# Optimization experiments

Hardware: AMD Instinct MI355X
Metric: run time of the kernel (lower is better)

Reference implementation:

```python
import jax, jax.numpy as jnp
import numpy as np

B, N, DEG, DIN, DM, H, DH, DO = 8, 4096, 16, 64, 128, 4, 32, 32
NLAYERS = 3
NN_SCALE = 1999853.335557038


def _layernorm(x, g, b, eps=1e-5):
    mu = jnp.mean(x, axis=-1, keepdims=True)
    var = jnp.var(x, axis=-1, keepdims=True)
    return (x - mu) * jax.lax.rsqrt(var + eps) * g + b


def setup_inputs() -> dict:
    key = jax.random.key(0)
    ks = jax.random.split(key, 24)
    s = 0.1
    inp = {
        'node_features': jax.random.normal(ks[0], (B, N, DIN), jnp.float32),
        'query_idxs': jax.random.randint(ks[1], (B,), 0, N, jnp.int32),
        'masks': (jax.random.uniform(ks[2], (B, N, DEG, 1)) > 0.2).astype(jnp.float32),
        'adj': jax.random.randint(ks[3], (B, N, DEG), 0, N, jnp.int32),
        'sim_results': jax.random.normal(ks[4], (B, 8), jnp.float32),
        'W0': jax.random.normal(ks[5], (DIN, DM), jnp.float32) * s,
        'b0': jnp.zeros((DM,), jnp.float32),
        'Wl': jax.random.normal(ks[6], (NLAYERS, H, DM, DH), jnp.float32) * s,
        'a_src': jax.random.normal(ks[7], (NLAYERS, H, DH), jnp.float32) * s,
        'a_dst': jax.random.normal(ks[8], (NLAYERS, H, DH), jnp.float32) * s,
        'Wo': jax.random.normal(ks[9], (NLAYERS, H, DH, DO), jnp.float32) * s,
        'Wlin': jax.random.normal(ks[10], (NLAYERS, H * DO, DM), jnp.float32) * s,
        'blin': jnp.zeros((NLAYERS, DM), jnp.float32),
        'ln_g': jnp.ones((NLAYERS, DM), jnp.float32),
        'ln_b': jnp.zeros((NLAYERS, DM), jnp.float32),
        'Wf1': jax.random.normal(ks[11], (DM, 256), jnp.float32) * s,
        'bf1': jnp.zeros((256,), jnp.float32),
        'Wf2': jax.random.normal(ks[12], (256, 128), jnp.float32) * s,
        'bf2': jnp.zeros((128,), jnp.float32),
        'Wf3': jax.random.normal(ks[13], (128, 8), jnp.float32) * s,
        'bf3': jnp.zeros((8,), jnp.float32),
    }
    return inp


def reference(node_features, query_idxs, masks, adj, sim_results,
              W0, b0, Wl, a_src, a_dst, Wo, Wlin, blin, ln_g, ln_b,
              Wf1, bf1, Wf2, bf2, Wf3, bf3):
    elu = jax.nn.elu
    x = elu(node_features @ W0 + b0)  # (B, N, DM)
    idx = adj.reshape(B, N * DEG, 1, 1)  # gather indices along node axis
    valid = masks > 0  # (B, N, DEG, 1)
    for l in range(NLAYERS):
        h = jnp.einsum('bnd,hdk->bnhk', x, Wl[l])  # (B, N, H, DH)
        hn = jnp.take_along_axis(h, idx, axis=1).reshape(B, N, DEG, H, DH)
        e_src = jnp.einsum('bnhk,hk->bnh', h, a_src[l])  # (B, N, H)
        e_dst = jnp.einsum('bnmhk,hk->bnmh', hn, a_dst[l])  # (B, N, DEG, H)
        e = jax.nn.leaky_relu(e_src[:, :, None, :] + e_dst, 0.2)
        e = jnp.where(valid, e, -1e9)
        alpha = jax.nn.softmax(e, axis=2)  # over neighbors
        agg = jnp.einsum('bnmh,bnmhk->bnhk', alpha, hn)  # (B, N, H, DH)
        out = jnp.einsum('bnhk,hko->bnho', agg, Wo[l]).reshape(B, N, H * DO)
        out = elu(out @ Wlin[l] + blin[l])  # AttnModule linear + ELU
        x = _layernorm(out + x, ln_g[l], ln_b[l])  # residual + LN
    qi = query_idxs.reshape(B, 1, 1)
    vnf = jnp.take_along_axis(x, qi, axis=1)[:, 0, :]  # (B, DM)
    vnf = elu(vnf @ Wf1 + bf1)
    vnf = elu(vnf @ Wf2 + bf2)
    vnf = elu(vnf @ Wf3 + bf3)
    return vnf * NN_SCALE
```

## Files before the change

### kernel.cpp

```cpp
#include <hip/hip_runtime.h>
#include <hip/hip_bf16.h>
#include <math.h>

#define BATCH 8
#define NNODE 4096
#define DEG 16
#define DIN 64
#define DM 128
#define NH 4
#define DHD 32
#define BN (BATCH*NNODE)
#define NLAYERS 3
#define NN_SCALE 1999853.335557038f

#define X_OFF     0
#define H_OFF     (BN*DM)
#define AGG_OFF   (2*BN*DM)
#define WLP_OFF   (3*BN*DM)
#define WCOMB_OFF (WLP_OFF + NLAYERS*DM*DM)

__device__ __forceinline__ float elu_f(float x) {
  return x > 0.f ? x : expm1f(x);
}

__global__ __launch_bounds__(256) void prep_kernel(
    const float* __restrict__ Wl, const float* __restrict__ Wo,
    const float* __restrict__ Wlin, float* __restrict__ ws) {
  const int bid = blockIdx.x;
  const int l = bid >> 4, sl = bid & 15;
  float* Wlp = ws + WLP_OFF   + l*DM*DM;
  float* Wcb = ws + WCOMB_OFF + l*DM*DM;
  const float* Wl_l   = Wl   + l*NH*DM*DHD;
  const float* Wo_l   = Wo   + l*NH*DHD*DHD;
  const float* Wlin_l = Wlin + l*DM*DM;
  for (int idx = sl*1024 + threadIdx.x; idx < (sl+1)*1024; idx += 256) {
    int d = idx >> 7, c = idx & 127;
    Wlp[idx] = Wl_l[((c>>5)*DM + d)*DHD + (c&31)];
  }
  for (int idx = sl*1024 + threadIdx.x; idx < (sl+1)*1024; idx += 256) {
    int r = idx >> 7, dcol = idx & 127;
    int h = r >> 5, k = r & 31;
    const float* wo  = Wo_l + (h*DHD + k)*DHD;
    const float* wl2 = Wlin_l + (h*DHD)*DM + dcol;
    float acc = 0.f;
    #pragma unroll
    for (int o = 0; o < DHD; o++) acc = fmaf(wo[o], wl2[o*DM], acc);
    Wcb[idx] = acc;
  }
}

template<int K, int EPI>
__global__ __launch_bounds__(128) void gemm_kernel(
    const float* __restrict__ A, const float* __restrict__ W,
    const float* __restrict__ bias, const float* __restrict__ lng,
    const float* __restrict__ lnb, const float* __restrict__ res,
    float* __restrict__ out) {
  __shared__ float xT[32][36];
  __shared__ float Wc[32][132];
  const int tid = threadIdx.x;
  const int j = tid & 15, i = tid >> 4;
  const int bid  = blockIdx.x;
  const int row0 = ((bid & 7) * 128 + (bid >> 3)) * 32;

  float acc[4][8];
  #pragma unroll
  for (int a = 0; a < 4; a++)
    #pragma unroll
    for (int b = 0; b < 8; b++) acc[a][b] = 0.f;

  float bval[8], gv[8], bv2[8];
  if (EPI != 0) {
    #pragma unroll
    for (int cc = 0; cc < 8; cc++) bval[cc] = bias[j*8 + cc];
  }
  if (EPI == 2) {
    #pragma unroll
    for (int cc = 0; cc < 8; cc++) { gv[cc] = lng[j*8+cc]; bv2[cc] = lnb[j*8+cc]; }
  }

  const int kq = tid & 7, rb = tid >> 3;

  float4 aR[2], wR[8];
  #pragma unroll
  for (int p = 0; p < 2; p++)
    aR[p] = *reinterpret_cast<const float4*>(
        &A[(size_t)(row0 + rb + p*16)*K + kq*4]);
  #pragma unroll
  for (int p = 0; p < 8; p++) {
    const int idx = p*128 + tid;
    const int d = idx >> 5, cq = idx & 31;
    wR[p] = *reinterpret_cast<const float4*>(&W[(size_t)d*128 + cq*4]);
  }

  for (int k0 = 0; k0 < K; k0 += 32) {
    __syncthreads();
    #pragma unroll
    for (int p = 0; p < 2; p++) {
      const int r = rb + p*16;
      xT[kq*4+0][r] = aR[p].x; xT[kq*4+1][r] = aR[p].y;
      xT[kq*4+2][r] = aR[p].z; xT[kq*4+3][r] = aR[p].w;
    }
    #pragma unroll
    for (int p = 0; p < 8; p++) {
      const int idx = p*128 + tid;
      const int d = idx >> 5, cq = idx & 31;
      *reinterpret_cast<float4*>(&Wc[d][cq*4]) = wR[p];
    }
    __syncthreads();
    if (k0 + 32 < K) {
      #pragma unroll
      for (int p = 0; p < 2; p++)
        aR[p] = *reinterpret_cast<const float4*>(
            &A[(size_t)(row0 + rb + p*16)*K + (k0 + 32) + kq*4]);
      #pragma unroll
      for (int p = 0; p < 8; p++) {
        const int idx = p*128 + tid;
        const int d = idx >> 5, cq = idx & 31;
        wR[p] = *reinterpret_cast<const float4*>(
            &W[(size_t)(k0 + 32 + d)*128 + cq*4]);
      }
    }
    #pragma unroll
    for (int kk = 0; kk < 32; kk++) {
      const float4 a0 = *reinterpret_cast<const float4*>(&xT[kk][i*4]);
      const float av[4] = {a0.x, a0.y, a0.z, a0.w};
      const float4 w0 = *reinterpret_cast<const float4*>(&Wc[kk][j*8]);
      const float4 w1 = *reinterpret_cast<const float4*>(&Wc[kk][j*8+4]);
      const float wv[8] = {w0.x,w0.y,w0.z,w0.w,w1.x,w1.y,w1.z,w1.w};
      #pragma unroll
      for (int rr = 0; rr < 4; rr++)
        #pragma unroll
        for (int cc = 0; cc < 8; cc++)
          acc[rr][cc] = fmaf(av[rr], wv[cc], acc[rr][cc]);
    }
  }

  if (EPI == 0) {
    #pragma unroll
    for (int rr = 0; rr < 4; rr++) {
      float* op = out + (size_t)(row0 + i*4 + rr)*DM + j*8;
      float4 v0 = {acc[rr][0],acc[rr][1],acc[rr][2],acc[rr][3]};
      float4 v1 = {acc[rr][4],acc[rr][5],acc[rr][6],acc[rr][7]};
      *reinterpret_cast<float4*>(op)     = v0;
      *reinterpret_cast<float4*>(op + 4) = v1;
    }
  } else if (EPI == 1) {
    #pragma unroll
    for (int rr = 0; rr < 4; rr++) {
      float* op = out + (size_t)(row0 + i*4 + rr)*DM + j*8;
      float4 v0, v1;
      v0.x = elu_f(acc[rr][0]+bval[0]); v0.y = elu_f(acc[rr][1]+bval[1]);
      v0.z = elu_f(acc[rr][2]+bval[2]); v0.w = elu_f(acc[rr][3]+bval[3]);
      v1.x = elu_f(acc[rr][4]+bval[4]); v1.y = elu_f(acc[rr][5]+bval[5]);
      v1.z = elu_f(acc[rr][6]+bval[6]); v1.w = elu_f(acc[rr][7]+bval[7]);
      *reinterpret_cast<float4*>(op)     = v0;
      *reinterpret_cast<float4*>(op + 4) = v1;
    }
  } else {
    float s[4], s2[4];
    #pragma unroll
    for (int rr = 0; rr < 4; rr++) {
      const int r = row0 + i*4 + rr;
      const float4 r0 = *reinterpret_cast<const float4*>(&res[(size_t)r*DM + j*8]);
      const float4 r1 = *reinterpret_cast<const float4*>(&res[(size_t)r*DM + j*8 + 4]);
      const float rv[8] = {r0.x,r0.y,r0.z,r0.w,r1.x,r1.y,r1.z,r1.w};
      s[rr] = 0.f; s2[rr] = 0.f;
      #pragma unroll
      for (int cc = 0; cc < 8; cc++) {
        float v = elu_f(acc[rr][cc] + bval[cc]) + rv[cc];
        acc[rr][cc] = v; s[rr] += v; s2[rr] += v*v;
      }
    }
    #pragma unroll
    for (int o = 1; o < 16; o <<= 1) {
      #pragma unroll
      for (int rr = 0; rr < 4; rr++) {
        s[rr]  += __shfl_xor(s[rr],  o);
        s2[rr] += __shfl_xor(s2[rr], o);
      }
    }
    #pragma unroll
    for (int rr = 0; rr < 4; rr++) {
      const int r = row0 + i*4 + rr;
      const float mu  = s[rr] * (1.f/128.f);
      const float var = s2[rr] * (1.f/128.f) - mu*mu;
      const float rs  = rsqrtf(var + 1e-5f);
      float4 v0, v1;
      v0.x = (acc[rr][0]-mu)*rs*gv[0] + bv2[0];
      v0.y = (acc[rr][1]-mu)*rs*gv[1] + bv2[1];
      v0.z = (acc[rr][2]-mu)*rs*gv[2] + bv2[2];
      v0.w = (acc[rr][3]-mu)*rs*gv[3] + bv2[3];
      v1.x = (acc[rr][4]-mu)*rs*gv[4] + bv2[4];
      v1.y = (acc[rr][5]-mu)*rs*gv[5] + bv2[5];
      v1.z = (acc[rr][6]-mu)*rs*gv[6] + bv2[6];
      v1.w = (acc[rr][7]-mu)*rs*gv[7] + bv2[7];
      float* op = out + (size_t)r*DM + j*8;
      *reinterpret_cast<float4*>(op)     = v0;
      *reinterpret_cast<float4*>(op + 4) = v1;
    }
  }
}

__global__ __launch_bounds__(256) void attn_kernel(
    const float* __restrict__ h, const int* __restrict__ adj,
    const float* __restrict__ masks, const float* __restrict__ a_src,
    const float* __restrict__ a_dst, float* __restrict__ agg) {
  const int lane = threadIdx.x & 63;
  const int wid  = threadIdx.x >> 6;
  const int bid  = blockIdx.x;
  const int node = ((bid & 7) << 12) + ((bid >> 3) << 2) + wid;
  const int b    = node >> 12;
  const int half = lane >> 5;
  const int c    = lane & 31;

  const float4 asr4 = *reinterpret_cast<const float4*>(a_src + 4*c);
  const float4 ad4  = *reinterpret_cast<const float4*>(a_dst + 4*c);

  const float4 hv = *reinterpret_cast<const float4*>(h + (size_t)node*DM + 4*c);
  float es = hv.x*asr4.x + hv.y*asr4.y + hv.z*asr4.z + hv.w*asr4.w;
  es += __shfl_xor(es, 1); es += __shfl_xor(es, 2); es += __shfl_xor(es, 4);

  float4 v[8]; float e[8];
  #pragma unroll
  for (int i = 0; i < 8; i++) {
    const int m  = 2*i + half;
    const int jn = adj[node*DEG + m];
    const float mval = masks[node*DEG + m];
    v[i] = *reinterpret_cast<const float4*>(
        h + ((size_t)(b*NNODE + jn))*DM + 4*c);
    float ed = v[i].x*ad4.x + v[i].y*ad4.y + v[i].z*ad4.z + v[i].w*ad4.w;
    ed += __shfl_xor(ed, 1); ed += __shfl_xor(ed, 2); ed += __shfl_xor(ed, 4);
    float t = es + ed;
    t = t > 0.f ? t : 0.2f*t;
    e[i] = (mval > 0.f) ? t : -1e9f;
  }

  float mx = e[0];
  #pragma unroll
  for (int i = 1; i < 8; i++) mx = fmaxf(mx, e[i]);
  mx = fmaxf(mx, __shfl_xor(mx, 32));
  float s = 0.f;
  #pragma unroll
  for (int i = 0; i < 8; i++) { e[i] = __expf(e[i] - mx); s += e[i]; }
  s += __shfl_xor(s, 32);
  const float inv = 1.f / s;

  float4 acc = {0.f, 0.f, 0.f, 0.f};
  #pragma unroll
  for (int i = 0; i < 8; i++) {
    const float a = e[i] * inv;
    acc.x = fmaf(a, v[i].x, acc.x); acc.y = fmaf(a, v[i].y, acc.y);
    acc.z = fmaf(a, v[i].z, acc.z); acc.w = fmaf(a, v[i].w, acc.w);
  }
  acc.x += __shfl_xor(acc.x, 32); acc.y += __shfl_xor(acc.y, 32);
  acc.z += __shfl_xor(acc.z, 32); acc.w += __shfl_xor(acc.w, 32);

  if (half == 0)
    *reinterpret_cast<float4*>(agg + (size_t)node*DM + 4*c) = acc;
}

__global__ __launch_bounds__(256) void mlp_kernel(
    const float* __restrict__ x, const int* __restrict__ qidx,
    const float* __restrict__ Wf1, const float* __restrict__ bf1,
    const float* __restrict__ Wf2, const float* __restrict__ bf2,
    const float* __restrict__ Wf3, const float* __restrict__ bf3,
    float* __restrict__ out) {
  __shared__ float xv[128];
  __shared__ float y1[256];
  __shared__ float y2[128];
  const int b = blockIdx.x, t = threadIdx.x;
  const int qi = qidx[b];
  if (t < 128) xv[t] = x[((size_t)b*NNODE + qi)*DM + t];
  __syncthreads();
  {
    float a1 = bf1[t];
    #pragma unroll 8
    for (int d = 0; d < 128; d++) a1 = fmaf(xv[d], Wf1[d*256 + t], a1);
    y1[t] = elu_f(a1);
  }
  __syncthreads();
  if (t < 128) {
    float a2 = bf2[t];
    #pragma unroll 8
    for (int d = 0; d < 256; d++) a2 = fmaf(y1[d], Wf2[d*128 + t], a2);
    y2[t] = elu_f(a2);
  }
  __syncthreads();
  if (t < 8) {
    float a3 = bf3[t];
    #pragma unroll 8
    for (int d = 0; d < 128; d++) a3 = fmaf(y2[d], Wf3[d*8 + t], a3);
    out[b*8 + t] = elu_f(a3) * NN_SCALE;
  }
}

extern "C" void kernel_launch(void* const* d_in, const int* in_sizes, int n_in,
                              void* d_out, int out_size, void* d_ws, size_t ws_size,
                              hipStream_t stream) {
  (void)in_sizes; (void)n_in; (void)out_size; (void)ws_size;
  const float* nf    = (const float*)d_in[0];
  const int*   qidx  = (const int*)d_in[1];
  const float* masks = (const float*)d_in[2];
  const int*   adj   = (const int*)d_in[3];
  const float* W0    = (const float*)d_in[5];
  const float* b0    = (const float*)d_in[6];
  const float* Wl    = (const float*)d_in[7];
  const float* a_src = (const float*)d_in[8];
  const float* a_dst = (const float*)d_in[9];
  const float* Wo    = (const float*)d_in[10];
  const float* Wlin  = (const float*)d_in[11];
  const float* blin  = (const float*)d_in[12];
  const float* ln_g  = (const float*)d_in[13];
  const float* ln_b  = (const float*)d_in[14];
  const float* Wf1   = (const float*)d_in[15];
  const float* bf1   = (const float*)d_in[16];
  const float* Wf2   = (const float*)d_in[17];
  const float* bf2   = (const float*)d_in[18];
  const float* Wf3   = (const float*)d_in[19];
  const float* bf3   = (const float*)d_in[20];

  float* ws  = (float*)d_ws;
  float* x   = ws + X_OFF;
  float* h   = ws + H_OFF;
  float* agg = ws + AGG_OFF;

  prep_kernel<<<48, 256, 0, stream>>>(Wl, Wo, Wlin, ws);

  gemm_kernel<DIN, 1><<<BN/32, 128, 0, stream>>>(
      nf, W0, b0, nullptr, nullptr, nullptr, x);

  for (int l = 0; l < NLAYERS; l++) {
    const float* Wlp = ws + WLP_OFF   + l*DM*DM;
    const float* Wcb = ws + WCOMB_OFF + l*DM*DM;
    gemm_kernel<DM, 0><<<BN/32, 128, 0, stream>>>(
        x, Wlp, nullptr, nullptr, nullptr, nullptr, h);
    attn_kernel<<<BN/4, 256, 0, stream>>>(
        h, adj, masks, a_src + l*NH*DHD, a_dst + l*NH*DHD, agg);
    gemm_kernel<DM, 2><<<BN/32, 128, 0, stream>>>(
        agg, Wcb, blin + l*DM, ln_g + l*DM, ln_b + l*DM, x, x);
  }

  mlp_kernel<<<8, 256, 0, stream>>>(
      x, qidx, Wf1, bf1, Wf2, bf2, Wf3, bf3, (float*)d_out);
}
```

Measured before the change: 402.5 us.

## Fuse attention aggregation with output GEMM, residual and layernorm

```diff
diff --git a/kernel.cpp b/kernel.cpp
--- a/kernel.cpp
+++ b/kernel.cpp
@@ -15,8 +15,7 @@
 
 #define X_OFF     0
 #define H_OFF     (BN*DM)
-#define AGG_OFF   (2*BN*DM)
-#define WLP_OFF   (3*BN*DM)
+#define WLP_OFF   (2*BN*DM)
 #define WCOMB_OFF (WLP_OFF + NLAYERS*DM*DM)
 
 __device__ __forceinline__ float elu_f(float x) {
@@ -52,9 +51,7 @@
 template<int K, int EPI>
 __global__ __launch_bounds__(128) void gemm_kernel(
     const float* __restrict__ A, const float* __restrict__ W,
-    const float* __restrict__ bias, const float* __restrict__ lng,
-    const float* __restrict__ lnb, const float* __restrict__ res,
-    float* __restrict__ out) {
+    const float* __restrict__ bias, float* __restrict__ out) {
   __shared__ float xT[32][36];
   __shared__ float Wc[32][132];
   const int tid = threadIdx.x;
@@ -68,14 +65,10 @@
     #pragma unroll
     for (int b = 0; b < 8; b++) acc[a][b] = 0.f;
 
-  float bval[8], gv[8], bv2[8];
+  float bval[8];
   if (EPI != 0) {
     #pragma unroll
     for (int cc = 0; cc < 8; cc++) bval[cc] = bias[j*8 + cc];
-  }
-  if (EPI == 2) {
-    #pragma unroll
-    for (int cc = 0; cc < 8; cc++) { gv[cc] = lng[j*8+cc]; bv2[cc] = lnb[j*8+cc]; }
   }
 
   const int kq = tid & 7, rb = tid >> 3;
@@ -135,128 +128,174 @@
     }
   }
 
-  if (EPI == 0) {
-    #pragma unroll
-    for (int rr = 0; rr < 4; rr++) {
-      float* op = out + (size_t)(row0 + i*4 + rr)*DM + j*8;
-      float4 v0 = {acc[rr][0],acc[rr][1],acc[rr][2],acc[rr][3]};
-      float4 v1 = {acc[rr][4],acc[rr][5],acc[rr][6],acc[rr][7]};
-      *reinterpret_cast<float4*>(op)     = v0;
-      *reinterpret_cast<float4*>(op + 4) = v1;
-    }
-  } else if (EPI == 1) {
-    #pragma unroll
-    for (int rr = 0; rr < 4; rr++) {
-      float* op = out + (size_t)(row0 + i*4 + rr)*DM + j*8;
-      float4 v0, v1;
+  #pragma unroll
+  for (int rr = 0; rr < 4; rr++) {
+    float* op = out + (size_t)(row0 + i*4 + rr)*DM + j*8;
+    float4 v0, v1;
+    if (EPI == 0) {
+      v0 = make_float4(acc[rr][0],acc[rr][1],acc[rr][2],acc[rr][3]);
+      v1 = make_float4(acc[rr][4],acc[rr][5],acc[rr][6],acc[rr][7]);
+    } else {
       v0.x = elu_f(acc[rr][0]+bval[0]); v0.y = elu_f(acc[rr][1]+bval[1]);
       v0.z = elu_f(acc[rr][2]+bval[2]); v0.w = elu_f(acc[rr][3]+bval[3]);
       v1.x = elu_f(acc[rr][4]+bval[4]); v1.y = elu_f(acc[rr][5]+bval[5]);
       v1.z = elu_f(acc[rr][6]+bval[6]); v1.w = elu_f(acc[rr][7]+bval[7]);
-      *reinterpret_cast<float4*>(op)     = v0;
-      *reinterpret_cast<float4*>(op + 4) = v1;
-    }
-  } else {
-    float s[4], s2[4];
-    #pragma unroll
-    for (int rr = 0; rr < 4; rr++) {
-      const int r = row0 + i*4 + rr;
-      const float4 r0 = *reinterpret_cast<const float4*>(&res[(size_t)r*DM + j*8]);
-      const float4 r1 = *reinterpret_cast<const float4*>(&res[(size_t)r*DM + j*8 + 4]);
-      const float rv[8] = {r0.x,r0.y,r0.z,r0.w,r1.x,r1.y,r1.z,r1.w};
-      s[rr] = 0.f; s2[rr] = 0.f;
-      #pragma unroll
-      for (int cc = 0; cc < 8; cc++) {
-        float v = elu_f(acc[rr][cc] + bval[cc]) + rv[cc];
-        acc[rr][cc] = v; s[rr] += v; s2[rr] += v*v;
-      }
-    }
-    #pragma unroll
-    for (int o = 1; o < 16; o <<= 1) {
-      #pragma unroll
-      for (int rr = 0; rr < 4; rr++) {
-        s[rr]  += __shfl_xor(s[rr],  o);
-        s2[rr] += __shfl_xor(s2[rr], o);
-      }
-    }
-    #pragma unroll
-    for (int rr = 0; rr < 4; rr++) {
-      const int r = row0 + i*4 + rr;
-      const float mu  = s[rr] * (1.f/128.f);
-      const float var = s2[rr] * (1.f/128.f) - mu*mu;
-      const float rs  = rsqrtf(var + 1e-5f);
-      float4 v0, v1;
-      v0.x = (acc[rr][0]-mu)*rs*gv[0] + bv2[0];
-      v0.y = (acc[rr][1]-mu)*rs*gv[1] + bv2[1];
-      v0.z = (acc[rr][2]-mu)*rs*gv[2] + bv2[2];
-      v0.w = (acc[rr][3]-mu)*rs*gv[3] + bv2[3];
-      v1.x = (acc[rr][4]-mu)*rs*gv[4] + bv2[4];
-      v1.y = (acc[rr][5]-mu)*rs*gv[5] + bv2[5];
-      v1.z = (acc[rr][6]-mu)*rs*gv[6] + bv2[6];
-      v1.w = (acc[rr][7]-mu)*rs*gv[7] + bv2[7];
-      float* op = out + (size_t)r*DM + j*8;
-      *reinterpret_cast<float4*>(op)     = v0;
-      *reinterpret_cast<float4*>(op + 4) = v1;
-    }
-  }
-}
-
-__global__ __launch_bounds__(256) void attn_kernel(
+    }
+    *reinterpret_cast<float4*>(op)     = v0;
+    *reinterpret_cast<float4*>(op + 4) = v1;
+  }
+}
+
+__global__ __launch_bounds__(256) void fused_attn_out_kernel(
     const float* __restrict__ h, const int* __restrict__ adj,
     const float* __restrict__ masks, const float* __restrict__ a_src,
-    const float* __restrict__ a_dst, float* __restrict__ agg) {
-  const int lane = threadIdx.x & 63;
-  const int wid  = threadIdx.x >> 6;
+    const float* __restrict__ a_dst, const float* __restrict__ Wcb,
+    const float* __restrict__ blin, const float* __restrict__ lng,
+    const float* __restrict__ lnb, float* __restrict__ x) {
+  __shared__ float agg_s[32][132];
+  __shared__ float Wc[32][132];
+  const int tid  = threadIdx.x;
   const int bid  = blockIdx.x;
-  const int node = ((bid & 7) << 12) + ((bid >> 3) << 2) + wid;
-  const int b    = node >> 12;
-  const int half = lane >> 5;
-  const int c    = lane & 31;
-
-  const float4 asr4 = *reinterpret_cast<const float4*>(a_src + 4*c);
-  const float4 ad4  = *reinterpret_cast<const float4*>(a_dst + 4*c);
-
-  const float4 hv = *reinterpret_cast<const float4*>(h + (size_t)node*DM + 4*c);
-  float es = hv.x*asr4.x + hv.y*asr4.y + hv.z*asr4.z + hv.w*asr4.w;
-  es += __shfl_xor(es, 1); es += __shfl_xor(es, 2); es += __shfl_xor(es, 4);
-
-  float4 v[8]; float e[8];
-  #pragma unroll
-  for (int i = 0; i < 8; i++) {
-    const int m  = 2*i + half;
-    const int jn = adj[node*DEG + m];
-    const float mval = masks[node*DEG + m];
-    v[i] = *reinterpret_cast<const float4*>(
-        h + ((size_t)(b*NNODE + jn))*DM + 4*c);
-    float ed = v[i].x*ad4.x + v[i].y*ad4.y + v[i].z*ad4.z + v[i].w*ad4.w;
-    ed += __shfl_xor(ed, 1); ed += __shfl_xor(ed, 2); ed += __shfl_xor(ed, 4);
-    float t = es + ed;
-    t = t > 0.f ? t : 0.2f*t;
-    e[i] = (mval > 0.f) ? t : -1e9f;
-  }
-
-  float mx = e[0];
-  #pragma unroll
-  for (int i = 1; i < 8; i++) mx = fmaxf(mx, e[i]);
-  mx = fmaxf(mx, __shfl_xor(mx, 32));
-  float s = 0.f;
-  #pragma unroll
-  for (int i = 0; i < 8; i++) { e[i] = __expf(e[i] - mx); s += e[i]; }
-  s += __shfl_xor(s, 32);
-  const float inv = 1.f / s;
-
-  float4 acc = {0.f, 0.f, 0.f, 0.f};
-  #pragma unroll
-  for (int i = 0; i < 8; i++) {
-    const float a = e[i] * inv;
-    acc.x = fmaf(a, v[i].x, acc.x); acc.y = fmaf(a, v[i].y, acc.y);
-    acc.z = fmaf(a, v[i].z, acc.z); acc.w = fmaf(a, v[i].w, acc.w);
-  }
-  acc.x += __shfl_xor(acc.x, 32); acc.y += __shfl_xor(acc.y, 32);
-  acc.z += __shfl_xor(acc.z, 32); acc.w += __shfl_xor(acc.w, 32);
-
-  if (half == 0)
-    *reinterpret_cast<float4*>(agg + (size_t)node*DM + 4*c) = acc;
+  const int node0 = ((bid & 7) * 128 + (bid >> 3)) * 32;
+  const int b     = node0 >> 12;
+
+  {
+    const int lane = tid & 63;
+    const int wid  = tid >> 6;
+    const int half = lane >> 5;
+    const int c    = lane & 31;
+    const float4 asr4 = *reinterpret_cast<const float4*>(a_src + 4*c);
+    const float4 ad4  = *reinterpret_cast<const float4*>(a_dst + 4*c);
+
+    for (int it = 0; it < 8; ++it) {
+      const int nl   = wid*8 + it;
+      const int node = node0 + nl;
+
+      const float4 hv = *reinterpret_cast<const float4*>(
+          h + (size_t)node*DM + 4*c);
+      float es = hv.x*asr4.x + hv.y*asr4.y + hv.z*asr4.z + hv.w*asr4.w;
+      es += __shfl_xor(es, 1); es += __shfl_xor(es, 2); es += __shfl_xor(es, 4);
+
+      float4 v[8]; float e[8];
+      #pragma unroll
+      for (int i = 0; i < 8; i++) {
+        const int m  = 2*i + half;
+        const int jn = adj[node*DEG + m];
+        const float mval = masks[node*DEG + m];
+        v[i] = *reinterpret_cast<const float4*>(
+            h + ((size_t)(b*NNODE + jn))*DM + 4*c);
+        float ed = v[i].x*ad4.x + v[i].y*ad4.y + v[i].z*ad4.z + v[i].w*ad4.w;
+        ed += __shfl_xor(ed, 1); ed += __shfl_xor(ed, 2); ed += __shfl_xor(ed, 4);
+        float t = es + ed;
+        t = t > 0.f ? t : 0.2f*t;
+        e[i] = (mval > 0.f) ? t : -1e9f;
+      }
+
+      float mx = e[0];
+      #pragma unroll
+      for (int i = 1; i < 8; i++) mx = fmaxf(mx, e[i]);
+      mx = fmaxf(mx, __shfl_xor(mx, 32));
+      float s = 0.f;
+      #pragma unroll
+      for (int i = 0; i < 8; i++) { e[i] = __expf(e[i] - mx); s += e[i]; }
+      s += __shfl_xor(s, 32);
+      const float inv = 1.f / s;
+
+      float4 acc = {0.f, 0.f, 0.f, 0.f};
+      #pragma unroll
+      for (int i = 0; i < 8; i++) {
+        const float a = e[i] * inv;
+        acc.x = fmaf(a, v[i].x, acc.x); acc.y = fmaf(a, v[i].y, acc.y);
+        acc.z = fmaf(a, v[i].z, acc.z); acc.w = fmaf(a, v[i].w, acc.w);
+      }
+      acc.x += __shfl_xor(acc.x, 32); acc.y += __shfl_xor(acc.y, 32);
+      acc.z += __shfl_xor(acc.z, 32); acc.w += __shfl_xor(acc.w, 32);
+
+      if (half == 0)
+        *reinterpret_cast<float4*>(&agg_s[nl][4*c]) = acc;
+    }
+  }
+  __syncthreads();
+
+  const int j = tid & 15, i = tid >> 4;
+  float bval[8], gv[8], bv2[8];
+  #pragma unroll
+  for (int cc = 0; cc < 8; cc++) {
+    bval[cc] = blin[j*8+cc]; gv[cc] = lng[j*8+cc]; bv2[cc] = lnb[j*8+cc];
+  }
+
+  float acc[2][8];
+  #pragma unroll
+  for (int a = 0; a < 2; a++)
+    #pragma unroll
+    for (int bb = 0; bb < 8; bb++) acc[a][bb] = 0.f;
+
+  for (int k0 = 0; k0 < DM; k0 += 32) {
+    __syncthreads();
+    #pragma unroll
+    for (int p = 0; p < 4; p++) {
+      const int idx = p*256 + tid;
+      const int d = idx >> 5, cq = idx & 31;
+      *reinterpret_cast<float4*>(&Wc[d][cq*4]) =
+          *reinterpret_cast<const float4*>(&Wcb[(size_t)(k0 + d)*128 + cq*4]);
+    }
+    __syncthreads();
+    #pragma unroll
+    for (int kk = 0; kk < 32; kk++) {
+      const float a0 = agg_s[i*2+0][k0+kk];
+      const float a1 = agg_s[i*2+1][k0+kk];
+      const float4 w0 = *reinterpret_cast<const float4*>(&Wc[kk][j*8]);
+      const float4 w1 = *reinterpret_cast<const float4*>(&Wc[kk][j*8+4]);
+      const float wv[8] = {w0.x,w0.y,w0.z,w0.w,w1.x,w1.y,w1.z,w1.w};
+      #pragma unroll
+      for (int cc = 0; cc < 8; cc++) {
+        acc[0][cc] = fmaf(a0, wv[cc], acc[0][cc]);
+        acc[1][cc] = fmaf(a1, wv[cc], acc[1][cc]);
+      }
+    }
+  }
+
+  float s[2], s2[2];
+  #pragma unroll
+  for (int rr = 0; rr < 2; rr++) {
+    const int r = node0 + i*2 + rr;
+    const float4 r0 = *reinterpret_cast<const float4*>(&x[(size_t)r*DM + j*8]);
+    const float4 r1 = *reinterpret_cast<const float4*>(&x[(size_t)r*DM + j*8 + 4]);
+    const float rv[8] = {r0.x,r0.y,r0.z,r0.w,r1.x,r1.y,r1.z,r1.w};
+    s[rr] = 0.f; s2[rr] = 0.f;
+    #pragma unroll
+    for (int cc = 0; cc < 8; cc++) {
+      float v = elu_f(acc[rr][cc] + bval[cc]) + rv[cc];
+      acc[rr][cc] = v; s[rr] += v; s2[rr] += v*v;
+    }
+  }
+  #pragma unroll
+  for (int o = 1; o < 16; o <<= 1) {
+    #pragma unroll
+    for (int rr = 0; rr < 2; rr++) {
+      s[rr]  += __shfl_xor(s[rr],  o);
+      s2[rr] += __shfl_xor(s2[rr], o);
+    }
+  }
+  #pragma unroll
+  for (int rr = 0; rr < 2; rr++) {
+    const int r = node0 + i*2 + rr;
+    const float mu  = s[rr] * (1.f/128.f);
+    const float var = s2[rr] * (1.f/128.f) - mu*mu;
+    const float rs  = rsqrtf(var + 1e-5f);
+    float4 v0, v1;
+    v0.x = (acc[rr][0]-mu)*rs*gv[0] + bv2[0];
+    v0.y = (acc[rr][1]-mu)*rs*gv[1] + bv2[1];
+    v0.z = (acc[rr][2]-mu)*rs*gv[2] + bv2[2];
+    v0.w = (acc[rr][3]-mu)*rs*gv[3] + bv2[3];
+    v1.x = (acc[rr][4]-mu)*rs*gv[4] + bv2[4];
+    v1.y = (acc[rr][5]-mu)*rs*gv[5] + bv2[5];
+    v1.z = (acc[rr][6]-mu)*rs*gv[6] + bv2[6];
+    v1.w = (acc[rr][7]-mu)*rs*gv[7] + bv2[7];
+    float* op = x + (size_t)r*DM + j*8;
+    *reinterpret_cast<float4*>(op)     = v0;
+    *reinterpret_cast<float4*>(op + 4) = v1;
+  }
 }
 
 __global__ __launch_bounds__(256) void mlp_kernel(
@@ -319,25 +358,21 @@
   const float* Wf3   = (const float*)d_in[19];
   const float* bf3   = (const float*)d_in[20];
 
-  float* ws  = (float*)d_ws;
-  float* x   = ws + X_OFF;
-  float* h   = ws + H_OFF;
-  float* agg = ws + AGG_OFF;
+  float* ws = (float*)d_ws;
+  float* x  = ws + X_OFF;
+  float* h  = ws + H_OFF;
 
   prep_kernel<<<48, 256, 0, stream>>>(Wl, Wo, Wlin, ws);
 
-  gemm_kernel<DIN, 1><<<BN/32, 128, 0, stream>>>(
-      nf, W0, b0, nullptr, nullptr, nullptr, x);
+  gemm_kernel<DIN, 1><<<BN/32, 128, 0, stream>>>(nf, W0, b0, x);
 
   for (int l = 0; l < NLAYERS; l++) {
     const float* Wlp = ws + WLP_OFF   + l*DM*DM;
     const float* Wcb = ws + WCOMB_OFF + l*DM*DM;
-    gemm_kernel<DM, 0><<<BN/32, 128, 0, stream>>>(
-        x, Wlp, nullptr, nullptr, nullptr, nullptr, h);
-    attn_kernel<<<BN/4, 256, 0, stream>>>(
-        h, adj, masks, a_src + l*NH*DHD, a_dst + l*NH*DHD, agg);
-    gemm_kernel<DM, 2><<<BN/32, 128, 0, stream>>>(
-        agg, Wcb, blin + l*DM, ln_g + l*DM, ln_b + l*DM, x, x);
+    gemm_kernel<DM, 0><<<BN/32, 128, 0, stream>>>(x, Wlp, nullptr, h);
+    fused_attn_out_kernel<<<BN/32, 256, 0, stream>>>(
+        h, adj, masks, a_src + l*NH*DHD, a_dst + l*NH*DHD,
+        Wcb, blin + l*DM, ln_g + l*DM, ln_b + l*DM, x);
   }
 
   mlp_kernel<<<8, 256, 0, stream>>>(
```

Measured after the change: 372.9 us. 1.08x faster.
